# Performance work log

Measured on AMD Instinct MI355X. Metric: run time of the kernel, lower is better.

The kernel has to match this reference:

```python
import jax, jax.numpy as jnp
import numpy as np

THRESHOLD = 0.9
EPS = 1e-12  # F.normalize eps


def setup_inputs() -> dict:
    key = jax.random.key(0)
    clusters = jax.random.normal(key, (64, 256, 768), dtype=jnp.float32)
    return {"clusters": clusters}


def _collapse(clusters, threshold):
    B, Q, D = clusters.shape
    # F.normalize(clusters, dim=-1): divide by L2 norm clamped to eps
    norm = jnp.maximum(jnp.linalg.norm(clusters, axis=-1, keepdims=True), EPS)
    nc = clusters / norm
    sim = jnp.einsum('bqd,bkd->bqk', nc, nc)              # [B, Q, Q]
    # torch loop condition: collapse_mask[:, i, j].any() -> any over batch
    pair_flag = jnp.any(sim > threshold, axis=0)          # [Q, Q] bool, fixed before merging

    # loop order: i outer, j inner (j > i) == row-major upper triangle
    ii, jj = jnp.triu_indices(Q, k=1)
    flags = pair_flag[ii, jj]                              # [Q*(Q-1)/2]

    def step(c, x):
        i, j, f = x
        ci = jnp.take(c, i, axis=1)                        # [B, D]
        cj = jnp.take(c, j, axis=1)
        new_i = jnp.where(f, (ci + cj) * 0.5, ci)
        c = c.at[:, i].set(new_i)
        c = c.at[:, j].set(jnp.where(f, new_i, cj))        # clusters[:, j] = clusters[:, i]
        return c, None

    out, _ = jax.lax.scan(step, clusters, (ii, jj, flags))
    return out


def reference(clusters):
    return _collapse(clusters, THRESHOLD)
```

## Files before the change

kernel.cpp:

```cpp
#include <hip/hip_runtime.h>
#include <math.h>

#define BB 64
#define QQ 256
#define DD 768
#define THR 0.9f
#define EPSN 1e-12f

#define OFF_FBITS  0
#define OFF_COUNT  8192
#define OFF_PAIRS  8320
#define OFF_M      138880

using f32x4 = __attribute__((ext_vector_type(4))) float;
using s16x8 = __attribute__((ext_vector_type(8))) short;

struct Frag { float4 lo, hi; };

#define GL2LDS(g, l) __builtin_amdgcn_global_load_lds( \
    (const __attribute__((address_space(1))) void*)(g), \
    (__attribute__((address_space(3))) void*)(l), 16, 0, 0)

__device__ __forceinline__ s16x8 cvt(const Frag& f) {
    union { s16x8 s; unsigned u[4]; } r;
    r.u[0] = __builtin_amdgcn_perm(__float_as_uint(f.lo.y), __float_as_uint(f.lo.x), 0x07060302u);
    r.u[1] = __builtin_amdgcn_perm(__float_as_uint(f.lo.w), __float_as_uint(f.lo.z), 0x07060302u);
    r.u[2] = __builtin_amdgcn_perm(__float_as_uint(f.hi.y), __float_as_uint(f.hi.x), 0x07060302u);
    r.u[3] = __builtin_amdgcn_perm(__float_as_uint(f.hi.w), __float_as_uint(f.hi.z), 0x07060302u);
    return r.s;
}
__device__ __forceinline__ float sq8(const Frag& f) {
    return f.lo.x*f.lo.x + f.lo.y*f.lo.y + f.lo.z*f.lo.z + f.lo.w*f.lo.w
         + f.hi.x*f.hi.x + f.hi.y*f.hi.y + f.hi.z*f.hi.z + f.hi.w*f.hi.w;
}

__global__ __launch_bounds__(256) void zero_kernel(unsigned* __restrict__ fbits,
                                                   int* __restrict__ count,
                                                   int* __restrict__ nflag) {
    int t = threadIdx.x;
    #pragma unroll
    for (int k = 0; k < 8; ++k) fbits[t + k * 256] = 0u;
    if (t == 0) { *count = 0; *nflag = 0; }
}

__global__ __launch_bounds__(256) void flags_kernel(const float* __restrict__ in,
                                                    float* __restrict__ out,
                                                    unsigned* __restrict__ fbits,
                                                    int* __restrict__ nflag) {
    __shared__ float lds[12288];

    int orig = blockIdx.x;
    int g = (orig & 7) * 80 + (orig >> 3);
    int tp = g % 10, b = g / 10;
    int it = 0, rem = tp, rowlen = 4;
    while (rem >= rowlen) { rem -= rowlen; ++it; --rowlen; }
    int jt = it + rem;
    int i0 = it * 64, j0 = jt * 64;

    int w = threadIdx.x >> 6, lane = threadIdx.x & 63;
    int wr = w >> 1, wc = w & 1;
    int r  = lane & 15, kg = lane >> 4;

    const float* base = in + (size_t)b * QQ * DD;

    int lr = lane >> 3;
    int lq = lane & 7;
    int swz = (lq ^ lr) * 4;
    const float* pA0 = base + (size_t)(i0 + w * 16 + lr) * DD + swz;
    const float* pA1 = pA0 + (size_t)8 * DD;
    const float* pB0 = base + (size_t)(j0 + w * 16 + lr) * DD + swz;
    const float* pB1 = pB0 + (size_t)8 * DD;

    f32x4 acc[2][2] = {};
    float4 ns = {0.f, 0.f, 0.f, 0.f};

    auto STAGE = [&](int buf, int c) {
        int k0 = c * 32;
        float* L = lds + buf * 4096 + w * 512;
        GL2LDS(pA0 + k0, L);
        GL2LDS(pA1 + k0, L + 256);
        GL2LDS(pB0 + k0, L + 2048);
        GL2LDS(pB1 + k0, L + 2048 + 256);
    };
    auto RD = [&](const float* L, int row) {
        int qlo = (2 * kg) ^ (row & 7);
        Frag f;
        f.lo = *(const float4*)&L[row * 32 + qlo * 4];
        f.hi = *(const float4*)&L[row * 32 + (qlo ^ 1) * 4];
        return f;
    };
    auto CHUNK = [&](int buf) {
        const float* LA = lds + buf * 4096;
        const float* LB = LA + 2048;
        Frag fa0 = RD(LA, wr * 32 + r);
        Frag fa1 = RD(LA, wr * 32 + r + 16);
        Frag fb0 = RD(LB, wc * 32 + r);
        Frag fb1 = RD(LB, wc * 32 + r + 16);
        ns.x += sq8(fa0); ns.y += sq8(fa1); ns.z += sq8(fb0); ns.w += sq8(fb1);
        s16x8 a0 = cvt(fa0), a1 = cvt(fa1), b0 = cvt(fb0), b1 = cvt(fb1);
        acc[0][0] = __builtin_amdgcn_mfma_f32_16x16x32_bf16(a0, b0, acc[0][0], 0, 0, 0);
        acc[0][1] = __builtin_amdgcn_mfma_f32_16x16x32_bf16(a0, b1, acc[0][1], 0, 0, 0);
        acc[1][0] = __builtin_amdgcn_mfma_f32_16x16x32_bf16(a1, b0, acc[1][0], 0, 0, 0);
        acc[1][1] = __builtin_amdgcn_mfma_f32_16x16x32_bf16(a1, b1, acc[1][1], 0, 0, 0);
    };

    STAGE(0, 0);
    STAGE(1, 1);
    #pragma unroll
    for (int c = 0; c < 24; ++c) {
        if (c + 2 < 24) STAGE((c + 2) % 3, c + 2);
        if (c <= 21)      asm volatile("s_waitcnt vmcnt(8)" ::: "memory");
        else if (c == 22) asm volatile("s_waitcnt vmcnt(4)" ::: "memory");
        else              asm volatile("s_waitcnt vmcnt(0)" ::: "memory");
        __builtin_amdgcn_s_barrier();
        CHUNK(c % 3);
        asm volatile("" ::: "memory");
        __builtin_amdgcn_s_barrier();
    }

    ns.x += __shfl_xor(ns.x, 16); ns.x += __shfl_xor(ns.x, 32);
    ns.y += __shfl_xor(ns.y, 16); ns.y += __shfl_xor(ns.y, 32);
    ns.z += __shfl_xor(ns.z, 16); ns.z += __shfl_xor(ns.z, 32);
    ns.w += __shfl_xor(ns.w, 16); ns.w += __shfl_xor(ns.w, 32);

    float njc0 = fmaxf(sqrtf(ns.z), EPSN);
    float njc1 = fmaxf(sqrtf(ns.w), EPSN);

    bool any = false;
    #pragma unroll
    for (int m = 0; m < 2; ++m) {
        float nsa = (m == 0) ? ns.x : ns.y;
        #pragma unroll
        for (int rr = 0; rr < 4; ++rr) {
            float ni2 = __shfl(nsa, kg * 4 + rr);
            float ni  = fmaxf(sqrtf(ni2), EPSN);
            int i = i0 + wr * 32 + m * 16 + kg * 4 + rr;
            int j = j0 + wc * 32 + r;
            if (j > i && acc[m][0][rr] > THR * ni * njc0) {
                int idx = i * QQ + j;
                atomicOr(&fbits[idx >> 5], 1u << (idx & 31)); any = true;
            }
            j += 16;
            if (j > i && acc[m][1][rr] > THR * ni * njc1) {
                int idx = i * QQ + j;
                atomicOr(&fbits[idx >> 5], 1u << (idx & 31)); any = true;
            }
        }
    }
    if (any) atomicAdd(nflag, 1);

    {
        const float4* s4 = (const float4*)in;
        float4* o4 = (float4*)out;
        const size_t N4 = (size_t)BB * QQ * DD / 4;
        for (size_t v = (size_t)orig * 256 + threadIdx.x; v < N4; v += (size_t)640 * 256)
            o4[v] = s4[v];
    }
}

__global__ __launch_bounds__(256) void compact_merge_kernel(const unsigned* __restrict__ fbits,
                                                            int* __restrict__ pairs,
                                                            int* __restrict__ count,
                                                            const int* __restrict__ nflag,
                                                            float* __restrict__ M) {
    int t = threadIdx.x;
    if (*nflag == 0) { if (t == 0) *count = 0; return; }

    const int P  = QQ * (QQ - 1) / 2;
    const int CH = (P + 255) / 256;
    int L0 = t * CH;
    int L1 = min(L0 + CH, P);

    int i = 0, cum = 0;
    while (i < QQ - 1 && cum + (QQ - 1 - i) <= L0) { cum += (QQ - 1 - i); ++i; }
    int j = i + 1 + (L0 - cum);

    auto getbit = [&](int ii, int jj) -> int {
        int idx = ii * QQ + jj;
        return (fbits[idx >> 5] >> (idx & 31)) & 1;
    };

    int cnt = 0;
    { int ii = i, jj = j;
      for (int L = L0; L < L1; ++L) {
          cnt += getbit(ii, jj);
          if (++jj == QQ) { ++ii; jj = ii + 1; }
      } }

    __shared__ int sc[256];
    sc[t] = cnt;
    __syncthreads();
    for (int off = 1; off < 256; off <<= 1) {
        int u = (t >= off) ? sc[t - off] : 0;
        __syncthreads();
        sc[t] += u;
        __syncthreads();
    }
    int bse = sc[t] - cnt;
    if (t == 255) *count = sc[255];

    { int ii = i, jj = j;
      for (int L = L0; L < L1; ++L) {
          if (getbit(ii, jj)) pairs[bse++] = (ii << 16) | jj;
          if (++jj == QQ) { ++ii; jj = ii + 1; }
      } }
    __syncthreads();

    int n = sc[255];
    for (int rr = 0; rr < QQ; ++rr) M[rr * QQ + t] = (rr == t) ? 1.f : 0.f;
    for (int s = 0; s < n; ++s) {
        int pr = pairs[s];
        int pi = pr >> 16, pj = pr & 0xffff;
        float nv = 0.5f * (M[pi * QQ + t] + M[pj * QQ + t]);
        M[pi * QQ + t] = nv;
        M[pj * QQ + t] = nv;
    }
}

__global__ __launch_bounds__(256) void applyM_kernel(const float* __restrict__ in,
                                                     const float* __restrict__ M,
                                                     float* __restrict__ out,
                                                     const int* __restrict__ count) {
    if (*count == 0) return;
    int b = blockIdx.x, qt = blockIdx.y;
    int t = threadIdx.x;
    for (int q = qt * 64; q < qt * 64 + 64; ++q) {
        float a0 = 0.f, a1 = 0.f, a2 = 0.f;
        for (int k = 0; k < QQ; ++k) {
            float m = M[q * QQ + k];
            if (m == 0.f) continue;
            const float* src = in + ((size_t)b * QQ + k) * DD;
            a0 += m * src[t];
            a1 += m * src[t + 256];
            a2 += m * src[t + 512];
        }
        float* dst = out + ((size_t)b * QQ + q) * DD;
        dst[t] = a0; dst[t + 256] = a1; dst[t + 512] = a2;
    }
}

extern "C" void kernel_launch(void* const* d_in, const int* in_sizes, int n_in,
                              void* d_out, int out_size, void* d_ws, size_t ws_size,
                              hipStream_t stream) {
    const float* in = (const float*)d_in[0];
    float* out = (float*)d_out;
    char* ws = (char*)d_ws;

    unsigned* fbits = (unsigned*)(ws + OFF_FBITS);
    int*   count = (int*)  (ws + OFF_COUNT);
    int*   nflag = (int*)  (ws + OFF_COUNT + 4);
    int*   pairs = (int*)  (ws + OFF_PAIRS);
    float* M     = (float*)(ws + OFF_M);

    zero_kernel<<<dim3(1), dim3(256), 0, stream>>>(fbits, count, nflag);
    flags_kernel<<<dim3(640), dim3(256), 0, stream>>>(in, out, fbits, nflag);
    compact_merge_kernel<<<dim3(1), dim3(256), 0, stream>>>(fbits, pairs, count, nflag, M);
    applyM_kernel<<<dim3(BB, 4), dim3(256), 0, stream>>>(in, M, out, count);
}
```

Before: 44.74 us.

## Interleave the input-to-output copy into the similarity GEMM pipeline

```diff
diff --git a/kernel.cpp b/kernel.cpp
--- a/kernel.cpp
+++ b/kernel.cpp
@@ -20,6 +20,8 @@
 #define GL2LDS(g, l) __builtin_amdgcn_global_load_lds( \
     (const __attribute__((address_space(1))) void*)(g), \
     (__attribute__((address_space(3))) void*)(l), 16, 0, 0)
+
+#define SCHED_FENCE() __builtin_amdgcn_sched_barrier(0)
 
 __device__ __forceinline__ s16x8 cvt(const Frag& f) {
     union { s16x8 s; unsigned u[4]; } r;
@@ -73,6 +75,19 @@
 
     f32x4 acc[2][2] = {};
     float4 ns = {0.f, 0.f, 0.f, 0.f};
+
+    const f32x4* in4 = (const f32x4*)in;
+    f32x4* out4 = (f32x4*)out;
+    f32x4 cr[3];
+    auto CLD = [&](int s) {
+        int off = tp * 24 + s; off = off < 192 ? off : 191;
+        cr[s % 3] = in4[(size_t)b * 49152 + (size_t)off * 256 + threadIdx.x];
+    };
+    auto CST = [&](int s) {
+        int off = tp * 24 + s; off = off < 192 ? off : 191;
+        __builtin_nontemporal_store(cr[s % 3],
+            &out4[(size_t)b * 49152 + (size_t)off * 256 + threadIdx.x]);
+    };
 
     auto STAGE = [&](int buf, int c) {
         int k0 = c * 32;
@@ -104,17 +119,24 @@
         acc[1][1] = __builtin_amdgcn_mfma_f32_16x16x32_bf16(a1, b1, acc[1][1], 0, 0, 0);
     };
 
-    STAGE(0, 0);
-    STAGE(1, 1);
+    CLD(0); STAGE(0, 0);
+    SCHED_FENCE();
+    CLD(1); STAGE(1, 1);
     #pragma unroll
     for (int c = 0; c < 24; ++c) {
-        if (c + 2 < 24) STAGE((c + 2) % 3, c + 2);
-        if (c <= 21)      asm volatile("s_waitcnt vmcnt(8)" ::: "memory");
-        else if (c == 22) asm volatile("s_waitcnt vmcnt(4)" ::: "memory");
-        else              asm volatile("s_waitcnt vmcnt(0)" ::: "memory");
+        SCHED_FENCE();
+        if (c < 22) { CLD(c + 2); STAGE((c + 2) % 3, c + 2); }
+        SCHED_FENCE();
+        if (c == 0)       asm volatile("s_waitcnt vmcnt(10)");
+        else if (c == 1)  asm volatile("s_waitcnt vmcnt(11)");
+        else if (c <= 21) asm volatile("s_waitcnt vmcnt(12)");
+        else if (c == 22) asm volatile("s_waitcnt vmcnt(7)");
+        else              asm volatile("s_waitcnt vmcnt(2)");
+        SCHED_FENCE();
         __builtin_amdgcn_s_barrier();
         CHUNK(c % 3);
-        asm volatile("" ::: "memory");
+        CST(c);
+        SCHED_FENCE();
         __builtin_amdgcn_s_barrier();
     }
 
@@ -148,14 +170,6 @@
         }
     }
     if (any) atomicAdd(nflag, 1);
-
-    {
-        const float4* s4 = (const float4*)in;
-        float4* o4 = (float4*)out;
-        const size_t N4 = (size_t)BB * QQ * DD / 4;
-        for (size_t v = (size_t)orig * 256 + threadIdx.x; v < N4; v += (size_t)640 * 256)
-            o4[v] = s4[v];
-    }
 }
 
 __global__ __launch_bounds__(256) void compact_merge_kernel(const unsigned* __restrict__ fbits,
```

New measurement: 38.00 us, median of 2. 15.1% less time.
